# Kernel optimization log

Hardware: AMD Instinct MI355X
Metric: run time of the kernel (lower is better)

## Reference

```python
import jax, jax.numpy as jnp
import numpy as np

HD = 64        # hidden_dim
H = 4          # heads
N = 50000      # nodes
E = 400000     # edges (before self loops)
NEG_ATT = 0.2  # GATConv attention LeakyReLU slope (PyG default)
NEG_ACT = 0.01 # nn.LeakyReLU() default slope
EPS = 1e-5     # BatchNorm eps


def _bn(x, gamma, beta):
    # training-mode BatchNorm1d over node dimension (biased variance)
    mu = x.mean(0)
    var = x.var(0)
    return gamma * (x - mu) * jax.lax.rsqrt(var + EPS) + beta


def _gatconv(h_in, src, dst, W, a_src, a_dst, bias, heads, outc, concat):
    n = h_in.shape[0]
    h = (h_in @ W.T).reshape(n, heads, outc)              # [N,H,C]
    al_s = jnp.einsum('nhc,hc->nh', h, a_src)             # [N,H]
    al_d = jnp.einsum('nhc,hc->nh', h, a_dst)
    e = jax.nn.leaky_relu(al_s[src] + al_d[dst], NEG_ATT) # [E',H]
    # softmax over incoming edges of each destination node
    m = jax.lax.stop_gradient(jax.ops.segment_max(e, dst, num_segments=n))
    ex = jnp.exp(e - m[dst])
    den = jax.ops.segment_sum(ex, dst, num_segments=n)
    alpha = ex / den[dst]                                  # [E',H]
    out = jax.ops.segment_sum(h[src] * alpha[..., None], dst, num_segments=n)
    out = out.reshape(n, heads * outc) if concat else out.mean(axis=1)
    return out + bias


def setup_inputs() -> dict:
    ks = jax.random.split(jax.random.key(0), 20)
    s = 0.1
    d = {
        'x': jax.random.normal(ks[0], (N, 2 * HD), jnp.float32),
        'edge_index': jax.random.randint(ks[1], (2, E), 0, N, jnp.int64),
        'W1': jax.random.normal(ks[2], (H * HD, 2 * HD), jnp.float32) * s,
        'a1s': jax.random.normal(ks[3], (H, HD), jnp.float32) * s,
        'a1d': jax.random.normal(ks[4], (H, HD), jnp.float32) * s,
        'b1': jnp.zeros((H * HD,), jnp.float32),
        'W2': jax.random.normal(ks[5], (H * HD, H * HD), jnp.float32) * s,
        'a2s': jax.random.normal(ks[6], (H, HD), jnp.float32) * s,
        'a2d': jax.random.normal(ks[7], (H, HD), jnp.float32) * s,
        'b2': jnp.zeros((H * HD,), jnp.float32),
        'W3': jax.random.normal(ks[8], (1 * HD, H * HD), jnp.float32) * s,
        'a3s': jax.random.normal(ks[9], (1, HD), jnp.float32) * s,
        'a3d': jax.random.normal(ks[10], (1, HD), jnp.float32) * s,
        'b3': jnp.zeros((HD,), jnp.float32),
        'gamma': jnp.ones((H * HD,), jnp.float32),
        'beta': jnp.zeros((H * HD,), jnp.float32),
    }
    return d


def reference(x, edge_index, W1, a1s, a1d, b1, W2, a2s, a2d, b2,
              W3, a3s, a3d, b3, gamma, beta):
    n = x.shape[0]
    loop = jnp.arange(n, dtype=edge_index.dtype)
    src = jnp.concatenate([edge_index[0], loop])  # add_self_loops=True
    dst = jnp.concatenate([edge_index[1], loop])

    h = _gatconv(x, src, dst, W1, a1s, a1d, b1, H, HD, True)
    h = jax.nn.leaky_relu(_bn(h, gamma, beta), NEG_ACT)

    # single middle residual block (num_layers=3); dropout is identity (eval)
    res = h
    h = _gatconv(h, src, dst, W2, a2s, a2d, b2, H, HD, True)
    h = jax.nn.leaky_relu(_bn(h, gamma, beta), NEG_ACT)
    h = h + res

    out = _gatconv(h, src, dst, W3, a3s, a3d, b3, 1, HD, False)
    return out
```

## Files before the change

kernel.cpp:

```cpp
#include <hip/hip_runtime.h>
#include <hip/hip_bf16.h>

#define NEG_ATT 0.2f
#define NEG_ACT 0.01f

typedef __attribute__((ext_vector_type(8))) short short8;
typedef __attribute__((ext_vector_type(4))) float f32x4;

__device__ __forceinline__ unsigned short f2bf(float f) {
    unsigned int u = __float_as_uint(f);
    unsigned int r = (u + 0x7fff + ((u >> 16) & 1)) >> 16;
    return (unsigned short)r;
}
__device__ __forceinline__ float b2f(unsigned short h) {
    return __uint_as_float((unsigned int)h << 16);
}


__global__ void init_deg(int* deg, int Nn) {
    int t = blockIdx.x * 256 + threadIdx.x;
    if (t < Nn) deg[t] = 1;
}

__global__ void count_edges(const int* __restrict__ ei, int* deg, int E) {
    int t = blockIdx.x * 256 + threadIdx.x;
    if (t < E) atomicAdd(&deg[ei[E + t]], 1);
}

#define SCAN_CHUNK 1024
__global__ void scan1(const int* __restrict__ deg, int* __restrict__ offs,
                      int* blocksum, int Nn) {
    __shared__ int sh[256];
    int b = blockIdx.x, t = threadIdx.x;
    int base = b * SCAN_CHUNK + t * 4;
    int v[4];
    int s = 0;
    for (int j = 0; j < 4; j++) {
        int idx = base + j;
        v[j] = (idx < Nn) ? deg[idx] : 0;
        s += v[j];
    }
    sh[t] = s;
    __syncthreads();
    for (int off = 1; off < 256; off <<= 1) {
        int x = (t >= off) ? sh[t - off] : 0;
        __syncthreads();
        sh[t] += x;
        __syncthreads();
    }
    int excl = sh[t] - s;
    if (t == 255) blocksum[b] = sh[255];
    int run = excl;
    for (int j = 0; j < 4; j++) {
        int idx = base + j;
        if (idx < Nn) offs[idx] = run;
        run += v[j];
    }
}

__global__ void scan2(int* blocksum, int G) {
    if (threadIdx.x == 0 && blockIdx.x == 0) {
        int run = 0;
        for (int i = 0; i < G; i++) { int v = blocksum[i]; blocksum[i] = run; run += v; }
    }
}

__global__ void scan3(int* offs, const int* base, int* cursor, int Nn, int total) {
    int i = blockIdx.x * 256 + threadIdx.x;
    if (i < Nn) {
        int v = offs[i] + base[i >> 10];
        offs[i] = v;
        cursor[i] = v;
    }
    if (i == 0) offs[Nn] = total;
}

__global__ void fill_csr(const int* __restrict__ ei, int* cursor, int* csr, int* dcsr,
                         int E, int Nn) {
    int t = blockIdx.x * 256 + threadIdx.x;
    if (t < E) {
        int s = ei[t];
        int d = ei[E + t];
        int p = atomicAdd(&cursor[d], 1);
        csr[p] = s;
        dcsr[p] = d;
    } else if (t < E + Nn) {
        int nn = t - E;
        int p = atomicAdd(&cursor[nn], 1);
        csr[p] = nn;
        dcsr[p] = nn;
    }
}


template <int HEADS>
__global__ __launch_bounds__(256) void edge_w(const int* __restrict__ csr,
                                              const int* __restrict__ dcsr,
                                              const float* __restrict__ als,
                                              const float* __restrict__ ald,
                                              float* __restrict__ wcsr, int Ep) {
    int t = blockIdx.x * 256 + threadIdx.x;
    if (t >= Ep) return;
    int s = csr[t], d = dcsr[t];
    if (HEADS == 4) {
        float4 a = *(const float4*)&als[s * 4];
        float4 b = *(const float4*)&ald[d * 4];
        float4 w;
        float e;
        e = a.x + b.x; e = e > 0.f ? e : NEG_ATT * e; w.x = __expf(e);
        e = a.y + b.y; e = e > 0.f ? e : NEG_ATT * e; w.y = __expf(e);
        e = a.z + b.z; e = e > 0.f ? e : NEG_ATT * e; w.z = __expf(e);
        e = a.w + b.w; e = e > 0.f ? e : NEG_ATT * e; w.w = __expf(e);
        *(float4*)&wcsr[(size_t)t * 4] = w;
    } else {
        float e = als[s] + ald[d];
        e = e > 0.f ? e : NEG_ATT * e;
        wcsr[t] = __expf(e);
    }
}


__global__ __launch_bounds__(256) void f2b8(const float* __restrict__ in,
                                            unsigned short* __restrict__ out,
                                            int n, int ntot) {
    int i = (blockIdx.x * 256 + threadIdx.x) * 8;
    if (i >= ntot) return;
    ushort4 lo, hi;
    if (i < n) {
        float4 a = *(const float4*)&in[i];
        float4 b = *(const float4*)&in[i + 4];
        lo = make_ushort4(f2bf(a.x), f2bf(a.y), f2bf(a.z), f2bf(a.w));
        hi = make_ushort4(f2bf(b.x), f2bf(b.y), f2bf(b.z), f2bf(b.w));
    } else {
        lo = make_ushort4(0, 0, 0, 0);
        hi = lo;
    }
    *(ushort4*)&out[i] = lo;
    *(ushort4*)&out[i + 4] = hi;
}

__global__ __launch_bounds__(256) void f2b_w3(const float* __restrict__ w1, unsigned short* o1, int n1,
                                              const float* __restrict__ w2, unsigned short* o2, int n2,
                                              const float* __restrict__ w3, unsigned short* o3, int n3) {
    int i = (blockIdx.x * 256 + threadIdx.x) * 8;
    const float* in;
    unsigned short* out;
    if (i < n1) { in = w1 + i; out = o1 + i; }
    else if (i < n1 + n2) { in = w2 + (i - n1); out = o2 + (i - n1); }
    else if (i < n1 + n2 + n3) { in = w3 + (i - n1 - n2); out = o3 + (i - n1 - n2); }
    else return;
    float4 a = *(const float4*)in;
    float4 b = *(const float4*)(in + 4);
    *(ushort4*)out = make_ushort4(f2bf(a.x), f2bf(a.y), f2bf(a.z), f2bf(a.w));
    *(ushort4*)(out + 4) = make_ushort4(f2bf(b.x), f2bf(b.y), f2bf(b.z), f2bf(b.w));
}


template <int K, int CO, int HEADS>
__global__ __launch_bounds__(256) void gemm_mfma(
    const unsigned short* __restrict__ Xb, const unsigned short* __restrict__ Wb,
    unsigned short* __restrict__ Hb, const float* __restrict__ a_s,
    const float* __restrict__ a_d, float* __restrict__ als, float* __restrict__ ald) {
    constexpr int BM = 128, BN = 64, BK = 64, LD = 72, SLD = 68;
    __shared__ __align__(16) char smem[4 * 32 * SLD * 4];
    unsigned short* As = (unsigned short*)smem;
    unsigned short* Bs = As + BM * LD;
    int tid = threadIdx.x;
    int wave = tid >> 6, lane = tid & 63;
    int quad = lane >> 4, l16 = lane & 15;
    int m0 = blockIdx.x * BM, n0 = blockIdx.y * BN;
    int hd = blockIdx.y;
    int arow = tid >> 3;
    int achk = (tid & 7) * 8;
    f32x4 acc[2][4] = {};
    for (int k0 = 0; k0 < K; k0 += BK) {
        __syncthreads();
#pragma unroll
        for (int p = 0; p < 4; p++) {
            int r = arow + p * 32;
            *(int4*)&As[r * LD + achk] = *(const int4*)&Xb[(size_t)(m0 + r) * K + k0 + achk];
        }
#pragma unroll
        for (int p = 0; p < 2; p++) {
            int r = arow + p * 32;
            *(int4*)&Bs[r * LD + achk] = *(const int4*)&Wb[(size_t)(n0 + r) * K + k0 + achk];
        }
        __syncthreads();
#pragma unroll
        for (int ks = 0; ks < 2; ks++) {
            short8 af[2], bfr[4];
#pragma unroll
            for (int i = 0; i < 2; i++)
                af[i] = *(const short8*)&As[(wave * 32 + i * 16 + l16) * LD + ks * 32 + quad * 8];
#pragma unroll
            for (int j = 0; j < 4; j++)
                bfr[j] = *(const short8*)&Bs[(j * 16 + l16) * LD + ks * 32 + quad * 8];
#pragma unroll
            for (int i = 0; i < 2; i++)
#pragma unroll
                for (int j = 0; j < 4; j++)
                    acc[i][j] = __builtin_amdgcn_mfma_f32_16x16x32_bf16(af[i], bfr[j], acc[i][j], 0, 0, 0);
        }
    }
    __syncthreads();

    float asv[4], adv[4];
#pragma unroll
    for (int j = 0; j < 4; j++) {
        asv[j] = a_s[hd * 64 + j * 16 + l16];
        adv[j] = a_d[hd * 64 + j * 16 + l16];
    }
#pragma unroll
    for (int i = 0; i < 2; i++)
#pragma unroll
        for (int r = 0; r < 4; r++) {
            float ps = acc[i][0][r] * asv[0] + acc[i][1][r] * asv[1] +
                       acc[i][2][r] * asv[2] + acc[i][3][r] * asv[3];
            float pd = acc[i][0][r] * adv[0] + acc[i][1][r] * adv[1] +
                       acc[i][2][r] * adv[2] + acc[i][3][r] * adv[3];
#pragma unroll
            for (int mm = 1; mm < 16; mm <<= 1) {
                ps += __shfl_xor(ps, mm);
                pd += __shfl_xor(pd, mm);
            }
            if (l16 == 0) {
                int m = m0 + wave * 32 + i * 16 + quad * 4 + r;
                als[m * HEADS + hd] = ps;
                ald[m * HEADS + hd] = pd;
            }
        }

    float* stg = (float*)smem + wave * 32 * SLD;
#pragma unroll
    for (int i = 0; i < 2; i++)
#pragma unroll
        for (int j = 0; j < 4; j++)
#pragma unroll
            for (int r = 0; r < 4; r++)
                stg[(i * 16 + quad * 4 + r) * SLD + j * 16 + l16] = acc[i][j][r];
    int g = lane >> 3, c8 = (lane & 7) * 8;
#pragma unroll
    for (int p = 0; p < 4; p++) {
        int row = p * 8 + g;
        float4 v0 = *(const float4*)&stg[row * SLD + c8];
        float4 v1 = *(const float4*)&stg[row * SLD + c8 + 4];
        uint4 o;
        o.x = ((unsigned)f2bf(v0.y) << 16) | f2bf(v0.x);
        o.y = ((unsigned)f2bf(v0.w) << 16) | f2bf(v0.z);
        o.z = ((unsigned)f2bf(v1.y) << 16) | f2bf(v1.x);
        o.w = ((unsigned)f2bf(v1.w) << 16) | f2bf(v1.z);
        *(uint4*)&Hb[(size_t)(m0 + wave * 32 + row) * CO + n0 + c8] = o;
    }
}


__global__ __launch_bounds__(256) void aggregate_h4(
    const unsigned short* __restrict__ Hb, const float* __restrict__ wcsr,
    const int* __restrict__ offs, const int* __restrict__ csr,
    const float* __restrict__ bias, float* __restrict__ Yout, int Nn) {
    int wave = threadIdx.x >> 6;
    int lane = threadIdx.x & 63;
    int n = blockIdx.x * 4 + wave;
    if (n >= Nn) return;
    int hd = lane >> 4;
    int c4 = lane * 4;
    int beg = offs[n], end = offs[n + 1];
    float4 acc = make_float4(0.f, 0.f, 0.f, 0.f);
    float den = 0.f;
    for (int b = beg; b < end; b += 64) {
        int cnt = min(64, end - b);
        int idx = 0;
        if (lane < cnt) idx = csr[b + lane];
        int j = 0;
        for (; j + 4 <= cnt; j += 4) {
            int s0 = __shfl(idx, j), s1 = __shfl(idx, j + 1);
            int s2 = __shfl(idx, j + 2), s3 = __shfl(idx, j + 3);
            float w0 = wcsr[(size_t)(b + j) * 4 + hd];
            float w1 = wcsr[(size_t)(b + j + 1) * 4 + hd];
            float w2 = wcsr[(size_t)(b + j + 2) * 4 + hd];
            float w3 = wcsr[(size_t)(b + j + 3) * 4 + hd];
            ushort4 h0 = *(const ushort4*)&Hb[(size_t)s0 * 256 + c4];
            ushort4 h1 = *(const ushort4*)&Hb[(size_t)s1 * 256 + c4];
            ushort4 h2 = *(const ushort4*)&Hb[(size_t)s2 * 256 + c4];
            ushort4 h3 = *(const ushort4*)&Hb[(size_t)s3 * 256 + c4];
            den += (w0 + w1) + (w2 + w3);
            acc.x += w0 * b2f(h0.x) + w1 * b2f(h1.x) + w2 * b2f(h2.x) + w3 * b2f(h3.x);
            acc.y += w0 * b2f(h0.y) + w1 * b2f(h1.y) + w2 * b2f(h2.y) + w3 * b2f(h3.y);
            acc.z += w0 * b2f(h0.z) + w1 * b2f(h1.z) + w2 * b2f(h2.z) + w3 * b2f(h3.z);
            acc.w += w0 * b2f(h0.w) + w1 * b2f(h1.w) + w2 * b2f(h2.w) + w3 * b2f(h3.w);
        }
        for (; j < cnt; j++) {
            int s = __shfl(idx, j);
            float w = wcsr[(size_t)(b + j) * 4 + hd];
            den += w;
            ushort4 hv = *(const ushort4*)&Hb[(size_t)s * 256 + c4];
            acc.x += w * b2f(hv.x); acc.y += w * b2f(hv.y);
            acc.z += w * b2f(hv.z); acc.w += w * b2f(hv.w);
        }
    }
    float inv = 1.f / den;
    float4 bv = *(const float4*)&bias[c4];
    float4 o = make_float4(acc.x * inv + bv.x, acc.y * inv + bv.y,
                           acc.z * inv + bv.z, acc.w * inv + bv.w);
    *(float4*)&Yout[(size_t)n * 256 + c4] = o;
}

__global__ __launch_bounds__(256) void aggregate_h1(
    const unsigned short* __restrict__ Hb, const float* __restrict__ wcsr,
    const int* __restrict__ offs, const int* __restrict__ csr,
    const float* __restrict__ bias, float* __restrict__ Yout, int Nn) {
    int wave = threadIdx.x >> 6;
    int lane = threadIdx.x & 63;
    int sub = lane >> 4, lane16 = lane & 15;
    int n = blockIdx.x * 16 + wave * 4 + sub;
    if (n >= Nn) return;
    int c4 = lane16 * 4;
    int beg = offs[n], end = offs[n + 1];
    float4 acc = make_float4(0.f, 0.f, 0.f, 0.f);
    float den = 0.f;
    for (int b = beg; b < end; b += 16) {
        int cnt = min(16, end - b);
        int idx = 0;
        if (lane16 < cnt) idx = csr[b + lane16];
        int j = 0;
        for (; j + 4 <= cnt; j += 4) {
            int s0 = __shfl(idx, (sub << 4) + j);
            int s1 = __shfl(idx, (sub << 4) + j + 1);
            int s2 = __shfl(idx, (sub << 4) + j + 2);
            int s3 = __shfl(idx, (sub << 4) + j + 3);
            float w0 = wcsr[b + j], w1 = wcsr[b + j + 1];
            float w2 = wcsr[b + j + 2], w3 = wcsr[b + j + 3];
            ushort4 h0 = *(const ushort4*)&Hb[(size_t)s0 * 64 + c4];
            ushort4 h1 = *(const ushort4*)&Hb[(size_t)s1 * 64 + c4];
            ushort4 h2 = *(const ushort4*)&Hb[(size_t)s2 * 64 + c4];
            ushort4 h3 = *(const ushort4*)&Hb[(size_t)s3 * 64 + c4];
            den += (w0 + w1) + (w2 + w3);
            acc.x += w0 * b2f(h0.x) + w1 * b2f(h1.x) + w2 * b2f(h2.x) + w3 * b2f(h3.x);
            acc.y += w0 * b2f(h0.y) + w1 * b2f(h1.y) + w2 * b2f(h2.y) + w3 * b2f(h3.y);
            acc.z += w0 * b2f(h0.z) + w1 * b2f(h1.z) + w2 * b2f(h2.z) + w3 * b2f(h3.z);
            acc.w += w0 * b2f(h0.w) + w1 * b2f(h1.w) + w2 * b2f(h2.w) + w3 * b2f(h3.w);
        }
        for (; j < cnt; j++) {
            int s = __shfl(idx, (sub << 4) + j);
            float w = wcsr[b + j];
            den += w;
            ushort4 hv = *(const ushort4*)&Hb[(size_t)s * 64 + c4];
            acc.x += w * b2f(hv.x); acc.y += w * b2f(hv.y);
            acc.z += w * b2f(hv.z); acc.w += w * b2f(hv.w);
        }
    }
    float inv = 1.f / den;
    float4 bv = *(const float4*)&bias[c4];
    float4 o = make_float4(acc.x * inv + bv.x, acc.y * inv + bv.y,
                           acc.z * inv + bv.z, acc.w * inv + bv.w);
    *(float4*)&Yout[(size_t)n * 64 + c4] = o;
}


__global__ __launch_bounds__(256) void bn_stats(const float* __restrict__ Y,
                                                float* __restrict__ partial, int Nn) {
    __shared__ float red[4 * 512];
    int t = threadIdx.x;
    int g = blockIdx.x;
    int rows_per = (Nn + gridDim.x - 1) / gridDim.x;
    int r0 = g * rows_per;
    int r1 = min(r0 + rows_per, Nn);
    int sub = t >> 6;
    int c4 = (t & 63) * 4;
    float4 s = make_float4(0.f, 0.f, 0.f, 0.f);
    float4 q = make_float4(0.f, 0.f, 0.f, 0.f);
    for (int r = r0 + sub; r < r1; r += 4) {
        float4 v = *(const float4*)&Y[(size_t)r * 256 + c4];
        s.x += v.x; s.y += v.y; s.z += v.z; s.w += v.w;
        q.x += v.x * v.x; q.y += v.y * v.y; q.z += v.z * v.z; q.w += v.w * v.w;
    }
    float* rs = &red[sub * 512];
    rs[c4 + 0] = s.x; rs[c4 + 1] = s.y; rs[c4 + 2] = s.z; rs[c4 + 3] = s.w;
    rs[256 + c4 + 0] = q.x; rs[256 + c4 + 1] = q.y;
    rs[256 + c4 + 2] = q.z; rs[256 + c4 + 3] = q.w;
    __syncthreads();
    float v0 = red[t] + red[512 + t] + red[1024 + t] + red[1536 + t];
    float v1 = red[256 + t] + red[768 + t] + red[1280 + t] + red[1792 + t];
    partial[(size_t)g * 512 + t] = v0;
    partial[(size_t)g * 512 + 256 + t] = v1;
}

__global__ __launch_bounds__(256) void bn_reduce_final(
    const float* __restrict__ partial, int NP, const float* __restrict__ gamma,
    const float* __restrict__ beta, float* scale, float* shift, int Nn) {
    __shared__ float sh[8];
    int ch = blockIdx.x;
    int t = threadIdx.x;
    int wave = t >> 6, lane = t & 63;
    float s = 0.f, q = 0.f;
    for (int i = t; i < NP; i += 256) {
        s += partial[(size_t)i * 512 + ch];
        q += partial[(size_t)i * 512 + 256 + ch];
    }
    for (int off = 32; off; off >>= 1) {
        s += __shfl_down(s, off);
        q += __shfl_down(q, off);
    }
    if (lane == 0) { sh[wave] = s; sh[4 + wave] = q; }
    __syncthreads();
    if (t == 0) {
        s = sh[0] + sh[1] + sh[2] + sh[3];
        q = sh[4] + sh[5] + sh[6] + sh[7];
        float inv_n = 1.f / (float)Nn;
        float mu = s * inv_n;
        float var = q * inv_n - mu * mu;
        float sc = gamma[ch] * rsqrtf(var + 1e-5f);
        scale[ch] = sc;
        shift[ch] = beta[ch] - mu * sc;
    }
}

template <bool RES, bool WF32>
__global__ __launch_bounds__(256) void bn_apply(const float* __restrict__ Y,
                                                const float* __restrict__ scale,
                                                const float* __restrict__ shift,
                                                const float* __restrict__ Res,
                                                float* __restrict__ Out,
                                                unsigned short* __restrict__ OutB,
                                                int total4, int total4pad) {
    int i = blockIdx.x * 256 + threadIdx.x;
    if (i >= total4pad) return;
    if (i >= total4) {
        *(ushort4*)&OutB[i * 4] = make_ushort4(0, 0, 0, 0);
        return;
    }
    float4 v = ((const float4*)Y)[i];
    int cb = (i * 4) & 255;
    float4 sc = *(const float4*)&scale[cb];
    float4 sh = *(const float4*)&shift[cb];
    float4 o;
    o.x = sc.x * v.x + sh.x; o.x = o.x > 0.f ? o.x : NEG_ACT * o.x;
    o.y = sc.y * v.y + sh.y; o.y = o.y > 0.f ? o.y : NEG_ACT * o.y;
    o.z = sc.z * v.z + sh.z; o.z = o.z > 0.f ? o.z : NEG_ACT * o.z;
    o.w = sc.w * v.w + sh.w; o.w = o.w > 0.f ? o.w : NEG_ACT * o.w;
    if (RES) {
        float4 r = ((const float4*)Res)[i];
        o.x += r.x; o.y += r.y; o.z += r.z; o.w += r.w;
    }
    if (WF32) ((float4*)Out)[i] = o;
    *(ushort4*)&OutB[i * 4] = make_ushort4(f2bf(o.x), f2bf(o.y), f2bf(o.z), f2bf(o.w));
}


extern "C" void kernel_launch(void* const* d_in, const int* in_sizes, int n_in,
                              void* d_out, int out_size, void* d_ws, size_t ws_size,
                              hipStream_t stream) {
    const float* x    = (const float*)d_in[0];
    const int*   ei   = (const int*)d_in[1];
    const float* W1   = (const float*)d_in[2];
    const float* a1s  = (const float*)d_in[3];
    const float* a1d  = (const float*)d_in[4];
    const float* b1   = (const float*)d_in[5];
    const float* W2   = (const float*)d_in[6];
    const float* a2s  = (const float*)d_in[7];
    const float* a2d  = (const float*)d_in[8];
    const float* b2   = (const float*)d_in[9];
    const float* W3   = (const float*)d_in[10];
    const float* a3s  = (const float*)d_in[11];
    const float* a3d  = (const float*)d_in[12];
    const float* b3   = (const float*)d_in[13];
    const float* gamma = (const float*)d_in[14];
    const float* beta  = (const float*)d_in[15];
    float* out = (float*)d_out;

    const int Nn = in_sizes[0] / 128;
    const int E  = in_sizes[1] / 2;
    const int Ep = E + Nn;
    const int Mpad = (Nn + 127) & ~127;

    size_t off = 0;
    char* base = (char*)d_ws;
    auto alloc = [&](size_t bytes) -> void* {
        void* p = base + off;
        off = (off + bytes + 255) & ~(size_t)255;
        return p;
    };
    unsigned short* Hb   = (unsigned short*)alloc((size_t)Mpad * 256 * 2);
    float* bufB   = (float*)alloc((size_t)Nn * 256 * 4);
    float* bufC   = (float*)alloc((size_t)Nn * 256 * 4);
    unsigned short* xb1  = (unsigned short*)alloc((size_t)Mpad * 128 * 2);
    unsigned short* xbig = (unsigned short*)alloc((size_t)Mpad * 256 * 2);
    unsigned short* wb1  = (unsigned short*)alloc((size_t)256 * 128 * 2);
    unsigned short* wb2  = (unsigned short*)alloc((size_t)256 * 256 * 2);
    unsigned short* wb3  = (unsigned short*)alloc((size_t)64 * 256 * 2);
    float* als    = (float*)alloc((size_t)Mpad * 4 * 4);
    float* ald    = (float*)alloc((size_t)Mpad * 4 * 4);
    int*   deg    = (int*)alloc((size_t)Nn * 4);
    int*   offs   = (int*)alloc((size_t)(Nn + 1) * 4);
    int*   cursor = (int*)alloc((size_t)Nn * 4);
    int*   bsum   = (int*)alloc(64 * 4);
    int*   csr    = (int*)alloc((size_t)Ep * 4);
    int*   dcsr   = (int*)alloc((size_t)Ep * 4);
    float* wcsr   = (float*)alloc((size_t)Ep * 4 * 4);
    const int NP = 1024;
    float* partial = (float*)alloc((size_t)NP * 512 * 4);
    float* scale  = (float*)alloc(256 * 4);
    float* shift  = (float*)alloc(256 * 4);
    (void)ws_size;

    const int G = (Nn + SCAN_CHUNK - 1) / SCAN_CHUNK;

    init_deg<<<(Nn + 255) / 256, 256, 0, stream>>>(deg, Nn);
    count_edges<<<(E + 255) / 256, 256, 0, stream>>>(ei, deg, E);
    scan1<<<G, 256, 0, stream>>>(deg, offs, bsum, Nn);
    scan2<<<1, 64, 0, stream>>>(bsum, G);
    scan3<<<(Nn + 255) / 256, 256, 0, stream>>>(offs, bsum, cursor, Nn, Ep);
    fill_csr<<<(Ep + 255) / 256, 256, 0, stream>>>(ei, cursor, csr, dcsr, E, Nn);

    {
        int ntot = Mpad * 128;
        f2b8<<<(ntot / 8 + 255) / 256, 256, 0, stream>>>(x, xb1, Nn * 128, ntot);
        int wtot = 256 * 128 + 256 * 256 + 64 * 256;
        f2b_w3<<<(wtot / 8 + 255) / 256, 256, 0, stream>>>(W1, wb1, 256 * 128,
                                                           W2, wb2, 256 * 256,
                                                           W3, wb3, 64 * 256);
    }

    const int gm = Mpad / 128;
    const int nagg4 = (Nn + 3) / 4;
    const int nagg1 = (Nn + 15) / 16;
    const int gedge = (Ep + 255) / 256;
    const int total4 = Nn * 64;
    const int total4pad = Mpad * 64;
    const int napply = (total4pad + 255) / 256;

    gemm_mfma<128, 256, 4><<<dim3(gm, 4), 256, 0, stream>>>(xb1, wb1, Hb, a1s, a1d, als, ald);
    edge_w<4><<<gedge, 256, 0, stream>>>(csr, dcsr, als, ald, wcsr, Ep);
    aggregate_h4<<<nagg4, 256, 0, stream>>>(Hb, wcsr, offs, csr, b1, bufB, Nn);
    bn_stats<<<NP, 256, 0, stream>>>(bufB, partial, Nn);
    bn_reduce_final<<<256, 256, 0, stream>>>(partial, NP, gamma, beta, scale, shift, Nn);
    bn_apply<false, true><<<napply, 256, 0, stream>>>(bufB, scale, shift, nullptr, bufC, xbig,
                                                      total4, total4pad);

    gemm_mfma<256, 256, 4><<<dim3(gm, 4), 256, 0, stream>>>(xbig, wb2, Hb, a2s, a2d, als, ald);
    edge_w<4><<<gedge, 256, 0, stream>>>(csr, dcsr, als, ald, wcsr, Ep);
    aggregate_h4<<<nagg4, 256, 0, stream>>>(Hb, wcsr, offs, csr, b2, bufB, Nn);
    bn_stats<<<NP, 256, 0, stream>>>(bufB, partial, Nn);
    bn_reduce_final<<<256, 256, 0, stream>>>(partial, NP, gamma, beta, scale, shift, Nn);
    bn_apply<true, false><<<napply, 256, 0, stream>>>(bufB, scale, shift, bufC, nullptr, xbig,
                                                      total4, total4pad);

    gemm_mfma<256, 64, 1><<<dim3(gm, 1), 256, 0, stream>>>(xbig, wb3, Hb, a3s, a3d, als, ald);
    edge_w<1><<<gedge, 256, 0, stream>>>(csr, dcsr, als, ald, wcsr, Ep);
    aggregate_h1<<<nagg1, 256, 0, stream>>>(Hb, wcsr, offs, csr, b3, out, Nn);
}
```

Before: 390.0 us.

## Fuse edge attention weights into aggregation and drop fp32 residual buffer

Computes the leaky-relu/exp attention weights inside the aggregation kernels from per-node als/ald, removing the separate edge_w kernels and the wcsr and dcsr edge arrays. It also merges the scan2/scan3 and bf16 conversion launches, and reads the residual from the bf16 activation buffer instead of a separate fp32 copy. This cuts edge-sized memory traffic and launch count. In exchange each edge does an extra scattered als gather and an exp, and the residual is rounded to bf16.

```diff
diff --git a/kernel.cpp b/kernel.cpp
--- a/kernel.cpp
+++ b/kernel.cpp
@@ -58,97 +58,61 @@
     }
 }
 
-__global__ void scan2(int* blocksum, int G) {
-    if (threadIdx.x == 0 && blockIdx.x == 0) {
-        int run = 0;
-        for (int i = 0; i < G; i++) { int v = blocksum[i]; blocksum[i] = run; run += v; }
-    }
-}
-
-__global__ void scan3(int* offs, const int* base, int* cursor, int Nn, int total) {
+__global__ void scan23(int* __restrict__ offs, const int* __restrict__ bsum,
+                       int* __restrict__ cursor, int Nn, int G) {
     int i = blockIdx.x * 256 + threadIdx.x;
-    if (i < Nn) {
-        int v = offs[i] + base[i >> 10];
-        offs[i] = v;
-        cursor[i] = v;
-    }
-    if (i == 0) offs[Nn] = total;
-}
-
-__global__ void fill_csr(const int* __restrict__ ei, int* cursor, int* csr, int* dcsr,
-                         int E, int Nn) {
+    if (i > Nn) return;
+    int g = i >> 10;
+    int basev = 0;
+    for (int k = 0; k < g; k++) basev += bsum[k];
+    if (i == Nn) {
+        int tot = basev;
+        for (int k = g; k < G; k++) tot += bsum[k];
+        offs[Nn] = tot;
+        return;
+    }
+    int v = offs[i] + basev;
+    offs[i] = v;
+    cursor[i] = v;
+}
+
+__global__ void fill_csr(const int* __restrict__ ei, int* cursor, int* csr, int E, int Nn) {
     int t = blockIdx.x * 256 + threadIdx.x;
     if (t < E) {
         int s = ei[t];
         int d = ei[E + t];
         int p = atomicAdd(&cursor[d], 1);
         csr[p] = s;
-        dcsr[p] = d;
     } else if (t < E + Nn) {
         int nn = t - E;
         int p = atomicAdd(&cursor[nn], 1);
         csr[p] = nn;
-        dcsr[p] = nn;
-    }
-}
-
-
-template <int HEADS>
-__global__ __launch_bounds__(256) void edge_w(const int* __restrict__ csr,
-                                              const int* __restrict__ dcsr,
-                                              const float* __restrict__ als,
-                                              const float* __restrict__ ald,
-                                              float* __restrict__ wcsr, int Ep) {
-    int t = blockIdx.x * 256 + threadIdx.x;
-    if (t >= Ep) return;
-    int s = csr[t], d = dcsr[t];
-    if (HEADS == 4) {
-        float4 a = *(const float4*)&als[s * 4];
-        float4 b = *(const float4*)&ald[d * 4];
-        float4 w;
-        float e;
-        e = a.x + b.x; e = e > 0.f ? e : NEG_ATT * e; w.x = __expf(e);
-        e = a.y + b.y; e = e > 0.f ? e : NEG_ATT * e; w.y = __expf(e);
-        e = a.z + b.z; e = e > 0.f ? e : NEG_ATT * e; w.z = __expf(e);
-        e = a.w + b.w; e = e > 0.f ? e : NEG_ATT * e; w.w = __expf(e);
-        *(float4*)&wcsr[(size_t)t * 4] = w;
-    } else {
-        float e = als[s] + ald[d];
-        e = e > 0.f ? e : NEG_ATT * e;
-        wcsr[t] = __expf(e);
-    }
-}
-
-
-__global__ __launch_bounds__(256) void f2b8(const float* __restrict__ in,
-                                            unsigned short* __restrict__ out,
-                                            int n, int ntot) {
-    int i = (blockIdx.x * 256 + threadIdx.x) * 8;
-    if (i >= ntot) return;
-    ushort4 lo, hi;
-    if (i < n) {
-        float4 a = *(const float4*)&in[i];
-        float4 b = *(const float4*)&in[i + 4];
-        lo = make_ushort4(f2bf(a.x), f2bf(a.y), f2bf(a.z), f2bf(a.w));
-        hi = make_ushort4(f2bf(b.x), f2bf(b.y), f2bf(b.z), f2bf(b.w));
-    } else {
-        lo = make_ushort4(0, 0, 0, 0);
-        hi = lo;
-    }
-    *(ushort4*)&out[i] = lo;
-    *(ushort4*)&out[i + 4] = hi;
-}
-
-__global__ __launch_bounds__(256) void f2b_w3(const float* __restrict__ w1, unsigned short* o1, int n1,
-                                              const float* __restrict__ w2, unsigned short* o2, int n2,
-                                              const float* __restrict__ w3, unsigned short* o3, int n3) {
+    }
+}
+
+
+__global__ __launch_bounds__(256) void f2b_all(
+    const float* __restrict__ x, unsigned short* __restrict__ xb, int nx, int nxpad,
+    const float* __restrict__ w1, unsigned short* __restrict__ o1, int n1,
+    const float* __restrict__ w2, unsigned short* __restrict__ o2, int n2,
+    const float* __restrict__ w3, unsigned short* __restrict__ o3, int n3) {
     int i = (blockIdx.x * 256 + threadIdx.x) * 8;
     const float* in;
     unsigned short* out;
-    if (i < n1) { in = w1 + i; out = o1 + i; }
-    else if (i < n1 + n2) { in = w2 + (i - n1); out = o2 + (i - n1); }
-    else if (i < n1 + n2 + n3) { in = w3 + (i - n1 - n2); out = o3 + (i - n1 - n2); }
-    else return;
+    if (i < nxpad) {
+        if (i >= nx) {
+            *(ushort4*)&xb[i] = make_ushort4(0, 0, 0, 0);
+            *(ushort4*)&xb[i + 4] = make_ushort4(0, 0, 0, 0);
+            return;
+        }
+        in = x + i; out = xb + i;
+    } else {
+        int j = i - nxpad;
+        if (j < n1) { in = w1 + j; out = o1 + j; }
+        else if (j < n1 + n2) { in = w2 + (j - n1); out = o2 + (j - n1); }
+        else if (j < n1 + n2 + n3) { in = w3 + (j - n1 - n2); out = o3 + (j - n1 - n2); }
+        else return;
+    }
     float4 a = *(const float4*)in;
     float4 b = *(const float4*)(in + 4);
     *(ushort4*)out = make_ushort4(f2bf(a.x), f2bf(a.y), f2bf(a.z), f2bf(a.w));
@@ -255,15 +219,17 @@
 
 
 __global__ __launch_bounds__(256) void aggregate_h4(
-    const unsigned short* __restrict__ Hb, const float* __restrict__ wcsr,
-    const int* __restrict__ offs, const int* __restrict__ csr,
-    const float* __restrict__ bias, float* __restrict__ Yout, int Nn) {
+    const unsigned short* __restrict__ Hb, const float* __restrict__ als,
+    const float* __restrict__ ald, const int* __restrict__ offs,
+    const int* __restrict__ csr, const float* __restrict__ bias,
+    float* __restrict__ Yout, int Nn) {
     int wave = threadIdx.x >> 6;
     int lane = threadIdx.x & 63;
     int n = blockIdx.x * 4 + wave;
     if (n >= Nn) return;
     int hd = lane >> 4;
     int c4 = lane * 4;
+    float aldn = ald[n * 4 + hd];
     int beg = offs[n], end = offs[n + 1];
     float4 acc = make_float4(0.f, 0.f, 0.f, 0.f);
     float den = 0.f;
@@ -275,14 +241,19 @@
         for (; j + 4 <= cnt; j += 4) {
             int s0 = __shfl(idx, j), s1 = __shfl(idx, j + 1);
             int s2 = __shfl(idx, j + 2), s3 = __shfl(idx, j + 3);
-            float w0 = wcsr[(size_t)(b + j) * 4 + hd];
-            float w1 = wcsr[(size_t)(b + j + 1) * 4 + hd];
-            float w2 = wcsr[(size_t)(b + j + 2) * 4 + hd];
-            float w3 = wcsr[(size_t)(b + j + 3) * 4 + hd];
+            float a0 = als[s0 * 4 + hd];
+            float a1 = als[s1 * 4 + hd];
+            float a2 = als[s2 * 4 + hd];
+            float a3 = als[s3 * 4 + hd];
             ushort4 h0 = *(const ushort4*)&Hb[(size_t)s0 * 256 + c4];
             ushort4 h1 = *(const ushort4*)&Hb[(size_t)s1 * 256 + c4];
             ushort4 h2 = *(const ushort4*)&Hb[(size_t)s2 * 256 + c4];
             ushort4 h3 = *(const ushort4*)&Hb[(size_t)s3 * 256 + c4];
+            float e0 = a0 + aldn; e0 = e0 > 0.f ? e0 : NEG_ATT * e0;
+            float e1 = a1 + aldn; e1 = e1 > 0.f ? e1 : NEG_ATT * e1;
+            float e2 = a2 + aldn; e2 = e2 > 0.f ? e2 : NEG_ATT * e2;
+            float e3 = a3 + aldn; e3 = e3 > 0.f ? e3 : NEG_ATT * e3;
+            float w0 = __expf(e0), w1 = __expf(e1), w2 = __expf(e2), w3 = __expf(e3);
             den += (w0 + w1) + (w2 + w3);
             acc.x += w0 * b2f(h0.x) + w1 * b2f(h1.x) + w2 * b2f(h2.x) + w3 * b2f(h3.x);
             acc.y += w0 * b2f(h0.y) + w1 * b2f(h1.y) + w2 * b2f(h2.y) + w3 * b2f(h3.y);
@@ -291,7 +262,9 @@
         }
         for (; j < cnt; j++) {
             int s = __shfl(idx, j);
-            float w = wcsr[(size_t)(b + j) * 4 + hd];
+            float e = als[s * 4 + hd] + aldn;
+            e = e > 0.f ? e : NEG_ATT * e;
+            float w = __expf(e);
             den += w;
             ushort4 hv = *(const ushort4*)&Hb[(size_t)s * 256 + c4];
             acc.x += w * b2f(hv.x); acc.y += w * b2f(hv.y);
@@ -306,15 +279,17 @@
 }
 
 __global__ __launch_bounds__(256) void aggregate_h1(
-    const unsigned short* __restrict__ Hb, const float* __restrict__ wcsr,
-    const int* __restrict__ offs, const int* __restrict__ csr,
-    const float* __restrict__ bias, float* __restrict__ Yout, int Nn) {
+    const unsigned short* __restrict__ Hb, const float* __restrict__ als,
+    const float* __restrict__ ald, const int* __restrict__ offs,
+    const int* __restrict__ csr, const float* __restrict__ bias,
+    float* __restrict__ Yout, int Nn) {
     int wave = threadIdx.x >> 6;
     int lane = threadIdx.x & 63;
     int sub = lane >> 4, lane16 = lane & 15;
     int n = blockIdx.x * 16 + wave * 4 + sub;
     if (n >= Nn) return;
     int c4 = lane16 * 4;
+    float aldn = ald[n];
     int beg = offs[n], end = offs[n + 1];
     float4 acc = make_float4(0.f, 0.f, 0.f, 0.f);
     float den = 0.f;
@@ -328,12 +303,16 @@
             int s1 = __shfl(idx, (sub << 4) + j + 1);
             int s2 = __shfl(idx, (sub << 4) + j + 2);
             int s3 = __shfl(idx, (sub << 4) + j + 3);
-            float w0 = wcsr[b + j], w1 = wcsr[b + j + 1];
-            float w2 = wcsr[b + j + 2], w3 = wcsr[b + j + 3];
+            float a0 = als[s0], a1 = als[s1], a2 = als[s2], a3 = als[s3];
             ushort4 h0 = *(const ushort4*)&Hb[(size_t)s0 * 64 + c4];
             ushort4 h1 = *(const ushort4*)&Hb[(size_t)s1 * 64 + c4];
             ushort4 h2 = *(const ushort4*)&Hb[(size_t)s2 * 64 + c4];
             ushort4 h3 = *(const ushort4*)&Hb[(size_t)s3 * 64 + c4];
+            float e0 = a0 + aldn; e0 = e0 > 0.f ? e0 : NEG_ATT * e0;
+            float e1 = a1 + aldn; e1 = e1 > 0.f ? e1 : NEG_ATT * e1;
+            float e2 = a2 + aldn; e2 = e2 > 0.f ? e2 : NEG_ATT * e2;
+            float e3 = a3 + aldn; e3 = e3 > 0.f ? e3 : NEG_ATT * e3;
+            float w0 = __expf(e0), w1 = __expf(e1), w2 = __expf(e2), w3 = __expf(e3);
             den += (w0 + w1) + (w2 + w3);
             acc.x += w0 * b2f(h0.x) + w1 * b2f(h1.x) + w2 * b2f(h2.x) + w3 * b2f(h3.x);
             acc.y += w0 * b2f(h0.y) + w1 * b2f(h1.y) + w2 * b2f(h2.y) + w3 * b2f(h3.y);
@@ -342,7 +321,9 @@
         }
         for (; j < cnt; j++) {
             int s = __shfl(idx, (sub << 4) + j);
-            float w = wcsr[b + j];
+            float e = als[s] + aldn;
+            e = e > 0.f ? e : NEG_ATT * e;
+            float w = __expf(e);
             den += w;
             ushort4 hv = *(const ushort4*)&Hb[(size_t)s * 64 + c4];
             acc.x += w * b2f(hv.x); acc.y += w * b2f(hv.y);
@@ -415,12 +396,10 @@
     }
 }
 
-template <bool RES, bool WF32>
+template <bool RES>
 __global__ __launch_bounds__(256) void bn_apply(const float* __restrict__ Y,
                                                 const float* __restrict__ scale,
                                                 const float* __restrict__ shift,
-                                                const float* __restrict__ Res,
-                                                float* __restrict__ Out,
                                                 unsigned short* __restrict__ OutB,
                                                 int total4, int total4pad) {
     int i = blockIdx.x * 256 + threadIdx.x;
@@ -439,10 +418,9 @@
     o.z = sc.z * v.z + sh.z; o.z = o.z > 0.f ? o.z : NEG_ACT * o.z;
     o.w = sc.w * v.w + sh.w; o.w = o.w > 0.f ? o.w : NEG_ACT * o.w;
     if (RES) {
-        float4 r = ((const float4*)Res)[i];
-        o.x += r.x; o.y += r.y; o.z += r.z; o.w += r.w;
-    }
-    if (WF32) ((float4*)Out)[i] = o;
+        ushort4 r = *(const ushort4*)&OutB[i * 4];
+        o.x += b2f(r.x); o.y += b2f(r.y); o.z += b2f(r.z); o.w += b2f(r.w);
+    }
     *(ushort4*)&OutB[i * 4] = make_ushort4(f2bf(o.x), f2bf(o.y), f2bf(o.z), f2bf(o.w));
 }
 
@@ -482,7 +460,6 @@
     };
     unsigned short* Hb   = (unsigned short*)alloc((size_t)Mpad * 256 * 2);
     float* bufB   = (float*)alloc((size_t)Nn * 256 * 4);
-    float* bufC   = (float*)alloc((size_t)Nn * 256 * 4);
     unsigned short* xb1  = (unsigned short*)alloc((size_t)Mpad * 128 * 2);
     unsigned short* xbig = (unsigned short*)alloc((size_t)Mpad * 256 * 2);
     unsigned short* wb1  = (unsigned short*)alloc((size_t)256 * 128 * 2);
@@ -495,8 +472,6 @@
     int*   cursor = (int*)alloc((size_t)Nn * 4);
     int*   bsum   = (int*)alloc(64 * 4);
     int*   csr    = (int*)alloc((size_t)Ep * 4);
-    int*   dcsr   = (int*)alloc((size_t)Ep * 4);
-    float* wcsr   = (float*)alloc((size_t)Ep * 4 * 4);
     const int NP = 1024;
     float* partial = (float*)alloc((size_t)NP * 512 * 4);
     float* scale  = (float*)alloc(256 * 4);
@@ -508,44 +483,35 @@
     init_deg<<<(Nn + 255) / 256, 256, 0, stream>>>(deg, Nn);
     count_edges<<<(E + 255) / 256, 256, 0, stream>>>(ei, deg, E);
     scan1<<<G, 256, 0, stream>>>(deg, offs, bsum, Nn);
-    scan2<<<1, 64, 0, stream>>>(bsum, G);
-    scan3<<<(Nn + 255) / 256, 256, 0, stream>>>(offs, bsum, cursor, Nn, Ep);
-    fill_csr<<<(Ep + 255) / 256, 256, 0, stream>>>(ei, cursor, csr, dcsr, E, Nn);
+    scan23<<<(Nn + 1 + 255) / 256, 256, 0, stream>>>(offs, bsum, cursor, Nn, G);
+    fill_csr<<<(Ep + 255) / 256, 256, 0, stream>>>(ei, cursor, csr, E, Nn);
 
     {
-        int ntot = Mpad * 128;
-        f2b8<<<(ntot / 8 + 255) / 256, 256, 0, stream>>>(x, xb1, Nn * 128, ntot);
+        int nxpad = Mpad * 128;
         int wtot = 256 * 128 + 256 * 256 + 64 * 256;
-        f2b_w3<<<(wtot / 8 + 255) / 256, 256, 0, stream>>>(W1, wb1, 256 * 128,
-                                                           W2, wb2, 256 * 256,
-                                                           W3, wb3, 64 * 256);
+        f2b_all<<<((nxpad + wtot) / 8 + 255) / 256, 256, 0, stream>>>(
+            x, xb1, Nn * 128, nxpad, W1, wb1, 256 * 128, W2, wb2, 256 * 256, W3, wb3, 64 * 256);
     }
 
     const int gm = Mpad / 128;
     const int nagg4 = (Nn + 3) / 4;
     const int nagg1 = (Nn + 15) / 16;
-    const int gedge = (Ep + 255) / 256;
     const int total4 = Nn * 64;
     const int total4pad = Mpad * 64;
     const int napply = (total4pad + 255) / 256;
 
     gemm_mfma<128, 256, 4><<<dim3(gm, 4), 256, 0, stream>>>(xb1, wb1, Hb, a1s, a1d, als, ald);
-    edge_w<4><<<gedge, 256, 0, stream>>>(csr, dcsr, als, ald, wcsr, Ep);
-    aggregate_h4<<<nagg4, 256, 0, stream>>>(Hb, wcsr, offs, csr, b1, bufB, Nn);
+    aggregate_h4<<<nagg4, 256, 0, stream>>>(Hb, als, ald, offs, csr, b1, bufB, Nn);
     bn_stats<<<NP, 256, 0, stream>>>(bufB, partial, Nn);
     bn_reduce_final<<<256, 256, 0, stream>>>(partial, NP, gamma, beta, scale, shift, Nn);
-    bn_apply<false, true><<<napply, 256, 0, stream>>>(bufB, scale, shift, nullptr, bufC, xbig,
-                                                      total4, total4pad);
+    bn_apply<false><<<napply, 256, 0, stream>>>(bufB, scale, shift, xbig, total4, total4pad);
 
     gemm_mfma<256, 256, 4><<<dim3(gm, 4), 256, 0, stream>>>(xbig, wb2, Hb, a2s, a2d, als, ald);
-    edge_w<4><<<gedge, 256, 0, stream>>>(csr, dcsr, als, ald, wcsr, Ep);
-    aggregate_h4<<<nagg4, 256, 0, stream>>>(Hb, wcsr, offs, csr, b2, bufB, Nn);
+    aggregate_h4<<<nagg4, 256, 0, stream>>>(Hb, als, ald, offs, csr, b2, bufB, Nn);
     bn_stats<<<NP, 256, 0, stream>>>(bufB, partial, Nn);
     bn_reduce_final<<<256, 256, 0, stream>>>(partial, NP, gamma, beta, scale, shift, Nn);
-    bn_apply<true, false><<<napply, 256, 0, stream>>>(bufB, scale, shift, bufC, nullptr, xbig,
-                                                      total4, total4pad);
+    bn_apply<true><<<napply, 256, 0, stream>>>(bufB, scale, shift, xbig, total4, total4pad);
 
     gemm_mfma<256, 64, 1><<<dim3(gm, 1), 256, 0, stream>>>(xbig, wb3, Hb, a3s, a3d, als, ald);
-    edge_w<1><<<gedge, 256, 0, stream>>>(csr, dcsr, als, ald, wcsr, Ep);
-    aggregate_h1<<<nagg1, 256, 0, stream>>>(Hb, wcsr, offs, csr, b3, out, Nn);
-}
+    aggregate_h1<<<nagg1, 256, 0, stream>>>(Hb, als, ald, offs, csr, b3, out, Nn);
+}
```

Measured after the change: 363.0 us. -6.9%, faster.
